# Kernel optimization log

Hardware: AMD Instinct MI355X
Metric: run time of the kernel (lower is better)

Reference implementation:

```python
import jax, jax.numpy as jnp
import numpy as np

N, H, T, L, D_IN, D_QK, D_V = 8, 8, 1024, 1024, 128, 128, 128


def setup_inputs() -> dict:
    key = jax.random.key(0)
    ks = jax.random.split(key, 12)
    s = 1.0 / np.sqrt(D_IN)
    sq = 1.0 / np.sqrt(D_QK)
    return {
        "X": jax.random.normal(ks[0], (N, H, L, D_IN), jnp.float32),
        "t1": jax.random.normal(ks[1], (N, T), jnp.float32),
        "Q": jax.random.normal(ks[2], (N, H, T, D_QK), jnp.float32),
        "Wk1": jax.random.normal(ks[3], (D_IN, D_QK), jnp.float32) * s,
        "bk1": jnp.zeros((D_QK,), jnp.float32),
        "Wk2": jax.random.normal(ks[4], (D_QK, D_QK), jnp.float32) * sq,
        "bk2": jnp.zeros((D_QK,), jnp.float32),
        "Wv1": jax.random.normal(ks[5], (D_IN, D_QK), jnp.float32) * s,
        "bv1": jnp.zeros((D_QK,), jnp.float32),
        "Wv2": jax.random.normal(ks[6], (D_QK, D_V), jnp.float32) * sq,
        "bv2": jnp.zeros((D_V,), jnp.float32),
        "log_tau": jnp.asarray(0.0, jnp.float32),  # log(init_tau=1)
    }


def _mlp(x, W1, b1, W2, b2):
    # MLP(d_in, [d_qk], d_out): Linear -> relu -> Linear
    return jax.nn.relu(x @ W1 + b1) @ W2 + b2


def reference(X, t1, Q, Wk1, bk1, Wk2, bk2, Wv1, bv1, Wv2, bv2, log_tau):
    t2 = X[:, 0, :, -1]                      # (N, L)
    K = _mlp(X, Wk1, bk1, Wk2, bk2)          # (N, H, L, d_qk)
    V = _mlp(X, Wv1, bv1, Wv2, bv2)          # (N, H, L, d_v)
    tau = jnp.exp(log_tau)
    # gaussian weight: -(Q.K)^2 / tau
    A = jnp.einsum('nhtc,nhlc->nhtl', Q, K)
    A = -(A * A) / tau
    mask = (t1[:, :, None] >= t2[:, None, :])[:, None, :, :]  # (N,1,T,L)
    A = jax.nn.softmax(A * mask, axis=-1) * mask
    return jnp.einsum('nhtl,nhlc->nhtc', A, V)
```

## Files before the change

### kernel.cpp

```cpp
#include <hip/hip_runtime.h>
#include <hip/hip_bf16.h>

typedef __bf16 bf16_t;
typedef _Float16 f16_t;
typedef bf16_t bf16x8 __attribute__((ext_vector_type(8)));
typedef f16_t  f16x8  __attribute__((ext_vector_type(8)));
typedef f16_t  f16x4  __attribute__((ext_vector_type(4)));
typedef float  floatx4 __attribute__((ext_vector_type(4)));
typedef float  floatx16 __attribute__((ext_vector_type(16)));
typedef bf16x8 bf16x8u __attribute__((aligned(8)));
typedef f16x8  f16x8u  __attribute__((aligned(8)));

#define DEV static __device__ __forceinline__

DEV floatx4 mfma16_bf16(bf16x8 a, bf16x8 b, floatx4 c) {
  return __builtin_amdgcn_mfma_f32_16x16x32_bf16(a, b, c, 0, 0, 0);
}
DEV floatx4 mfma16_f16(f16x8 a, f16x8 b, floatx4 c) {
  return __builtin_amdgcn_mfma_f32_16x16x32_f16(a, b, c, 0, 0, 0);
}
DEV floatx16 mfma32_bf16(bf16x8 a, bf16x8 b, floatx16 c) {
  return __builtin_amdgcn_mfma_f32_32x32x16_bf16(a, b, c, 0, 0, 0);
}
DEV floatx16 mfma32x8_f16(f16x4 a, f16x4 b, floatx16 c) {
  return __builtin_amdgcn_mfma_f32_32x32x8f16(a, b, c, 0, 0, 0);
}
DEV void async_ld16(void* lds, const void* g) {
  __builtin_amdgcn_global_load_lds(
      (const __attribute__((address_space(1))) unsigned int*)g,
      (__attribute__((address_space(3))) unsigned int*)lds, 16, 0, 0);
}
DEV float fast_exp2(float x) {
  float r;
  asm("v_exp_f32 %0, %1" : "=v"(r) : "v"(x));
  return r;
}

__global__ void prep_kernel(const float* __restrict__ Wk1, const float* __restrict__ Wk2,
                            const float* __restrict__ Wv1, const float* __restrict__ Wv2,
                            const float* __restrict__ X,
                            bf16_t* __restrict__ W1p, bf16_t* __restrict__ W2p,
                            f16_t* __restrict__ W3f, f16_t* __restrict__ W4f,
                            float* __restrict__ t2pre) {
  int b = blockIdx.x;
  if (b < 16) {
    int m = b >> 2, p = b & 3;
    const float* src = m == 0 ? Wk1 : m == 1 ? Wk2 : m == 2 ? Wv1 : Wv2;
    __shared__ float tile[32][129];
    for (int u = 0; u < 4; ++u) {
      int idx = threadIdx.x + u * 256;
      int k = idx >> 5, n4 = (idx & 31) << 2;
      float4 v = *(const float4*)(src + (size_t)(p * 32 + k) * 128 + n4);
      tile[k][n4 + 0] = v.x; tile[k][n4 + 1] = v.y;
      tile[k][n4 + 2] = v.z; tile[k][n4 + 3] = v.w;
    }
    __syncthreads();
    if (m < 2) {
      bf16_t* dst = m ? W2p : W1p;
      for (int u = 0; u < 2; ++u) {
        int idx = threadIdx.x + u * 256;
        int n = idx >> 2, kc = idx & 3;
        bf16x8 hi, lo;
        for (int j = 0; j < 8; ++j) {
          float v = tile[kc * 8 + j][n];
          bf16_t hh = (bf16_t)v;
          hi[j] = hh;
          lo[j] = (bf16_t)(v - (float)hh);
        }
        *(bf16x8*)(dst + n * 128 + p * 32 + kc * 8) = hi;
        *(bf16x8*)(dst + 16384 + n * 128 + p * 32 + kc * 8) = lo;
      }
    } else {
      f16_t* dst = (m == 3) ? W4f : W3f;
      for (int u = 0; u < 2; ++u) {
        int idx = threadIdx.x + u * 256;
        int n = idx >> 2, kc = idx & 3;
        f16x8 w;
        for (int j = 0; j < 8; ++j) w[j] = (f16_t)tile[kc * 8 + j][n];
        *(f16x8*)(dst + n * 128 + p * 32 + kc * 8) = w;
      }
    }
  } else {
    int i = (b - 16) * 256 + threadIdx.x;
    t2pre[i] = X[((size_t)(i >> 10) * 8192 + (i & 1023)) * 128 + 127];
  }
}

__global__ __launch_bounds__(256) void mlp_k_kernel(
    const float* __restrict__ X, const float* __restrict__ b1,
    const float* __restrict__ b2, const bf16_t* __restrict__ W1p,
    const bf16_t* __restrict__ W2p, bf16_t* __restrict__ Khi,
    bf16_t* __restrict__ Klo) {
  __shared__ __align__(16) char sXbuf[2 * 16896];
  __shared__ __align__(16) bf16_t sW[2][256 * 40];
  bf16_t* sXh = (bf16_t*)sXbuf;
  bf16_t* sXl = sXh + 64 * 132;

  const int tid = threadIdx.x, lane = tid & 63, wave = tid >> 6;
  const int q = lane >> 4, c15 = lane & 15;
  const size_t rowBase = (size_t)blockIdx.x * 64;

  int goff[5];
  for (int a = 0; a < 5; ++a) {
    int o = (wave + 4 * a) * 1024 + lane * 16;
    int row = o / 80, rem = o % 80;
    goff[a] = row * 256 + (rem < 64 ? rem : 0);
  }
  auto issueW = [&](int buf, int ph) {
    const bf16_t* Wp = (ph < 4) ? W1p : W2p;
    const char* base = (const char*)Wp + (ph & 3) * 64;
    for (int a = 0; a < 5; ++a)
      async_ld16((char*)sW[buf] + (wave + 4 * a) * 1024 + lane * 16, base + goff[a]);
  };

  issueW(0, 0);

  float b1v[8], b2v[8];
  for (int nt = 0; nt < 8; ++nt) { b1v[nt] = b1[nt * 16 + c15]; b2v[nt] = b2[nt * 16 + c15]; }

  for (int u = 0; u < 8; ++u) {
    int idx = tid + u * 256;
    int r = idx >> 5, c4 = (idx & 31) << 2;
    float4 v = *(const float4*)(X + (rowBase + r) * 128 + c4);
    int o = r * 132 + c4;
    float vv[4] = {v.x, v.y, v.z, v.w};
    for (int i = 0; i < 4; ++i) {
      bf16_t h = (bf16_t)vv[i];
      sXh[o + i] = h;
      sXl[o + i] = (bf16_t)(vv[i] - (float)h);
    }
  }

  floatx4 acc1[8], acc2[8];
  for (int i = 0; i < 8; ++i) { acc1[i] = {}; acc2[i] = {}; }

  __syncthreads();
#pragma unroll
  for (int ph = 0; ph < 8; ++ph) {
    if (ph < 7) issueW((ph + 1) & 1, ph + 1);
    const bf16_t* wb = sW[ph & 1];
    const int kq = ph & 3;
    floatx4* acc = (ph < 4) ? acc1 : acc2;
    const int ao = (wave * 16 + c15) * 132 + kq * 32 + q * 8;
    bf16x8 ah = *(const bf16x8u*)(sXh + ao);
    bf16x8 al = *(const bf16x8u*)(sXl + ao);
    for (int nt = 0; nt < 8; ++nt) {
      const int bo = (nt * 16 + c15) * 40 + q * 8;
      bf16x8 bh = *(const bf16x8*)(wb + bo);
      bf16x8 bl = *(const bf16x8*)(wb + 128 * 40 + bo);
      acc[nt] = mfma16_bf16(ah, bh, acc[nt]);
      acc[nt] = mfma16_bf16(ah, bl, acc[nt]);
      acc[nt] = mfma16_bf16(al, bh, acc[nt]);
    }
    if (ph == 3) {
      for (int nt = 0; nt < 8; ++nt)
        for (int r = 0; r < 4; ++r) {
          float h = fmaxf(acc1[nt][r] + b1v[nt], 0.f);
          bf16_t hh = (bf16_t)h;
          int o = (wave * 16 + q * 4 + r) * 132 + nt * 16 + c15;
          sXh[o] = hh;
          sXl[o] = (bf16_t)(h - (float)hh);
        }
    }
    __syncthreads();
  }

  for (int nt = 0; nt < 8; ++nt)
    for (int r = 0; r < 4; ++r) {
      float kv = acc2[nt][r] + b2v[nt];
      bf16_t kh = (bf16_t)kv;
      int o = (wave * 16 + q * 4 + r) * 132 + nt * 16 + c15;
      sXh[o] = kh;
      sXl[o] = (bf16_t)(kv - (float)kh);
    }
  __syncthreads();
  for (int u = 0; u < 4; ++u) {
    int idx = tid + u * 256;
    int r = idx >> 4, c8 = (idx & 15) << 3;
    bf16x8 vh = *(const bf16x8u*)(sXh + r * 132 + c8);
    bf16x8 vl = *(const bf16x8u*)(sXl + r * 132 + c8);
    *(bf16x8*)(Khi + (rowBase + r) * 128 + c8) = vh;
    *(bf16x8*)(Klo + (rowBase + r) * 128 + c8) = vl;
  }
}

__global__ __launch_bounds__(256) void mlp_v_kernel(
    const float* __restrict__ X, const float* __restrict__ b1,
    const float* __restrict__ b2, const f16_t* __restrict__ W1f,
    const f16_t* __restrict__ W2f, f16_t* __restrict__ Vt) {
  __shared__ __align__(16) f16_t sXf[64 * 136];
  __shared__ __align__(16) f16_t sW[2][128 * 40];

  const int tid = threadIdx.x, lane = tid & 63, wave = tid >> 6;
  const int q = lane >> 4, c15 = lane & 15;
  const size_t rowBase = (size_t)blockIdx.x * 64;

  int goff[3];
  for (int a = 0; a < 3; ++a) {
    int o = (wave + 4 * a) * 1024 + lane * 16;
    int row = o / 80, rem = o % 80;
    goff[a] = row * 256 + (rem < 64 ? rem : 0);
  }
  auto issueV = [&](int buf, int ph) {
    const f16_t* Wp = (ph < 4) ? W1f : W2f;
    const char* base = (const char*)Wp + (ph & 3) * 64;
    for (int a = 0; a < 3; ++a) {
      int j = wave + 4 * a;
      if (j < 10) async_ld16((char*)sW[buf] + j * 1024 + lane * 16, base + goff[a]);
    }
  };

  issueV(0, 0);

  float b1v[8], bvv[2][4];
  for (int nt = 0; nt < 8; ++nt) b1v[nt] = b1[nt * 16 + c15];
  for (int mt = 0; mt < 2; ++mt)
    for (int r = 0; r < 4; ++r)
      bvv[mt][r] = b2[(wave * 2 + mt) * 16 + q * 4 + r];

  for (int u = 0; u < 8; ++u) {
    int idx = tid + u * 256;
    int r = idx >> 5, c4 = (idx & 31) << 2;
    float4 v = *(const float4*)(X + (rowBase + r) * 128 + c4);
    int o = r * 136 + c4;
    sXf[o + 0] = (f16_t)v.x; sXf[o + 1] = (f16_t)v.y;
    sXf[o + 2] = (f16_t)v.z; sXf[o + 3] = (f16_t)v.w;
  }

  floatx4 acc1[8], acc2[2][4];
  for (int i = 0; i < 8; ++i) acc1[i] = {};
  for (int i = 0; i < 2; ++i) for (int j = 0; j < 4; ++j) acc2[i][j] = {};

  __syncthreads();
#pragma unroll
  for (int ph = 0; ph < 8; ++ph) {
    if (ph < 7) issueV((ph + 1) & 1, ph + 1);
    const f16_t* wb = sW[ph & 1];
    const int kq = ph & 3;
    if (ph < 4) {
      f16x8 a = *(const f16x8u*)(sXf + (wave * 16 + c15) * 136 + kq * 32 + q * 8);
      for (int nt = 0; nt < 8; ++nt) {
        f16x8 bb = *(const f16x8*)(wb + (nt * 16 + c15) * 40 + q * 8);
        acc1[nt] = mfma16_f16(a, bb, acc1[nt]);
      }
      if (ph == 3) {
        for (int nt = 0; nt < 8; ++nt)
          for (int r = 0; r < 4; ++r)
            sXf[(wave * 16 + q * 4 + r) * 136 + nt * 16 + c15] =
                (f16_t)fmaxf(acc1[nt][r] + b1v[nt], 0.f);
      }
    } else {
      f16x8 aw0 = *(const f16x8*)(wb + ((wave * 2 + 0) * 16 + c15) * 40 + q * 8);
      f16x8 aw1 = *(const f16x8*)(wb + ((wave * 2 + 1) * 16 + c15) * 40 + q * 8);
      for (int nt = 0; nt < 4; ++nt) {
        f16x8 bh = *(const f16x8u*)(sXf + (nt * 16 + c15) * 136 + kq * 32 + q * 8);
        acc2[0][nt] = mfma16_f16(aw0, bh, acc2[0][nt]);
        acc2[1][nt] = mfma16_f16(aw1, bh, acc2[1][nt]);
      }
    }
    __syncthreads();
  }

  f16_t* sVT = sXf;
  for (int mt = 0; mt < 2; ++mt)
    for (int nt = 0; nt < 4; ++nt)
      for (int r = 0; r < 4; ++r) {
        int c = (wave * 2 + mt) * 16 + q * 4 + r;
        sVT[c * 68 + nt * 16 + c15] = (f16_t)(acc2[mt][nt][r] + bvv[mt][r]);
      }
  __syncthreads();
  const int nh = (int)(rowBase >> 10);
  const int lB = (int)(rowBase & 1023);
  for (int u = 0; u < 4; ++u) {
    int idx = tid + u * 256;
    int c = idx >> 3, l8 = (idx & 7) << 3;
    *(f16x8*)(Vt + ((size_t)nh * 128 + c) * 1024 + lB + l8) =
        *(const f16x8u*)(sVT + c * 68 + l8);
  }
}

__global__ __launch_bounds__(256, 2) void attn_kernel(
    const float* __restrict__ Q, const float* __restrict__ t1,
    const float* __restrict__ t2pre, const float* __restrict__ ltau,
    const bf16_t* __restrict__ Khi, const bf16_t* __restrict__ Klo,
    const f16_t* __restrict__ Vt, float* __restrict__ out) {
  __shared__ __align__(16) char sBuf[3][24576];
  __shared__ __align__(16) float sT2[1024];

  const int tid = threadIdx.x, lane = tid & 63, wave = tid >> 6;
  const int h = lane >> 5, l31 = lane & 31;
  const int nh = blockIdx.x & 63;
  const int seg = blockIdx.x >> 6;
  const int n = nh >> 3;
  const int qrow = seg * 128 + wave * 32 + l31;
  const float negc2 = -__expf(-ltau[0]) * 1.44269504f;
  const int vswz = (l31 >> 1) & 3;

  const char* gp[6]; int ls[6]; int st[6];
  for (int a = 0; a < 6; ++a) {
    int j = wave + 4 * a;
    if (j < 16) {
      int o = j * 1024 + lane * 16;
      int half = o >> 13;
      int r2 = o & 8191;
      int row = r2 >> 8;
      int s = (r2 >> 4) & 15;
      int g = s ^ (row & 15);
      gp[a] = (const char*)(half ? Klo : Khi) +
              ((size_t)((nh << 10) + row)) * 256 + (g << 4);
      st[a] = 8192; ls[a] = o;
    } else {
      int o = (j - 16) * 1024 + lane * 16;
      int c = o >> 6;
      int u = (o >> 4) & 3;
      int up = u ^ ((c >> 1) & 3);
      gp[a] = (const char*)Vt + ((size_t)((nh << 7) + c)) * 2048 + up * 16;
      st[a] = 64; ls[a] = 16384 + o;
    }
  }
  auto stage = [&](int buf) {
    for (int a = 0; a < 6; ++a) { async_ld16(sBuf[buf] + ls[a], gp[a]); gp[a] += st[a]; }
  };

  float4 t2v4 = *(const float4*)(t2pre + (n << 10) + tid * 4);
  const float t1v = t1[(n << 10) + qrow];
  bf16x8 qh[8], ql[8];
  {
    const float* qr = Q + ((size_t)(nh << 10) + qrow) * 128;
    for (int ks = 0; ks < 8; ++ks) {
      const float* p = qr + ks * 16 + h * 8;
      float4 v0 = *(const float4*)p;
      float4 v1 = *(const float4*)(p + 4);
      float vv[8] = {v0.x, v0.y, v0.z, v0.w, v1.x, v1.y, v1.z, v1.w};
      bf16x8 hi, lo;
      for (int j = 0; j < 8; ++j) {
        bf16_t hj = (bf16_t)vv[j];
        hi[j] = hj;
        lo[j] = (bf16_t)(vv[j] - (float)hj);
      }
      qh[ks] = hi;
      ql[ks] = lo;
    }
  }
  stage(0);
  stage(1);
  *(float4*)(sT2 + tid * 4) = t2v4;

  floatx16 O[4];
  for (int i = 0; i < 4; ++i) O[i] = {};
  float ds = 0.f;

  asm volatile("s_waitcnt vmcnt(6) lgkmcnt(0)" ::: "memory");
  __builtin_amdgcn_s_barrier();
  asm volatile("" ::: "memory");

  for (int it = 0; it < 32; ++it) {
    if (it <= 29) stage((it + 2) % 3);
    const char* kb = sBuf[it % 3];
    const char* vb = kb + 16384;

    floatx16 S = {};
    __builtin_amdgcn_s_setprio(1);
#pragma unroll
    for (int ks = 0; ks < 8; ++ks) {
      const int bo = l31 * 256 + ((((ks << 1) + h) ^ (l31 & 15)) << 4);
      bf16x8 kh_ = *(const bf16x8*)(kb + bo);
      bf16x8 kl_ = *(const bf16x8*)(kb + 8192 + bo);
      S = mfma32_bf16(kh_, qh[ks], S);
      S = mfma32_bf16(kl_, qh[ks], S);
      S = mfma32_bf16(kh_, ql[ks], S);
    }
    __builtin_amdgcn_s_setprio(0);

    const float* t2b = sT2 + it * 32 + h * 4;
    for (int t = 0; t < 4; ++t) {
      float4 tv4 = *(const float4*)(t2b + t * 8);
      float tv[4] = {tv4.x, tv4.y, tv4.z, tv4.w};
      f16x4 pb;
      for (int j = 0; j < 4; ++j) {
        float s = S[4 * t + j];
        float e = fast_exp2(s * s * negc2);
        bool m = (t1v >= tv[j]);
        ds += m ? e : 1.f;
        pb[j] = (f16_t)(m ? e : 0.f);
      }
      for (int ct = 0; ct < 4; ++ct) {
        f16x4 va = *(const f16x4*)(vb + (ct * 32 + l31) * 64 +
                                   ((t ^ vswz) << 4) + h * 8);
        O[ct] = mfma32x8_f16(va, pb, O[ct]);
      }
    }

    if (it <= 29) {
      asm volatile("s_waitcnt vmcnt(6)" ::: "memory");
    } else if (it == 30) {
      asm volatile("s_waitcnt vmcnt(0)" ::: "memory");
    }
    if (it < 31) {
      asm volatile("" ::: "memory");
      __builtin_amdgcn_s_barrier();
      asm volatile("" ::: "memory");
    }
  }

  ds += __shfl_xor(ds, 32);
  const float inv = 1.f / ds;
  float* orow = out + ((size_t)(nh << 10) + qrow) * 128;
  for (int ct = 0; ct < 4; ++ct)
    for (int t = 0; t < 4; ++t) {
      int c = ct * 32 + 8 * t + 4 * h;
      float4 v = {O[ct][4 * t + 0] * inv, O[ct][4 * t + 1] * inv,
                  O[ct][4 * t + 2] * inv, O[ct][4 * t + 3] * inv};
      *(float4*)(orow + c) = v;
    }
}

extern "C" void kernel_launch(void* const* d_in, const int* in_sizes, int n_in,
                              void* d_out, int out_size, void* d_ws, size_t ws_size,
                              hipStream_t stream) {
  const float* X   = (const float*)d_in[0];
  const float* t1  = (const float*)d_in[1];
  const float* Q   = (const float*)d_in[2];
  const float* Wk1 = (const float*)d_in[3];
  const float* bk1 = (const float*)d_in[4];
  const float* Wk2 = (const float*)d_in[5];
  const float* bk2 = (const float*)d_in[6];
  const float* Wv1 = (const float*)d_in[7];
  const float* bv1 = (const float*)d_in[8];
  const float* Wv2 = (const float*)d_in[9];
  const float* bv2 = (const float*)d_in[10];
  const float* log_tau = (const float*)d_in[11];
  float* out = (float*)d_out;

  const size_t E = (size_t)64 * 1024 * 128;
  bf16_t* Khi = (bf16_t*)d_ws;
  bf16_t* Klo = Khi + E;
  f16_t*  Vt  = (f16_t*)(Klo + E);
  bf16_t* W1p = (bf16_t*)((char*)d_ws + 3 * E * 2);
  bf16_t* W2p = W1p + 32768;
  f16_t*  W3f = (f16_t*)(W2p + 32768);
  f16_t*  W4f = W3f + 16384;
  float*  t2pre = (float*)(W4f + 16384);

  prep_kernel<<<48, 256, 0, stream>>>(Wk1, Wk2, Wv1, Wv2, X, W1p, W2p, W3f, W4f, t2pre);
  mlp_k_kernel<<<1024, 256, 0, stream>>>(X, bk1, bk2, W1p, W2p, Khi, Klo);
  mlp_v_kernel<<<1024, 256, 0, stream>>>(X, bv1, bv2, W3f, W4f, Vt);
  attn_kernel<<<512, 256, 0, stream>>>(Q, t1, t2pre, log_tau, Khi, Klo, Vt, out);
}
```

Before: 230.3 us.

## Switch attention kernel to 16x16 MFMA tiles with 8 waves per block

The attention kernel moves from 32x32 MFMA tiles (one 32-query tile per wave, 4 waves) to 16x16 MFMA tiles (16 queries per wave, 8 waves per 512-thread block). The async staging work is spread across 8 waves with 3 loads each, and the V LDS swizzle is changed to match the new access pattern. Launch bounds change to 512 threads with a target of 4 blocks. The aim is more waves per CU to hide latency and smaller per-wave accumulators. The cost is more LDS reads of K and V per MFMA, since each 16x16 tile gets less operand reuse.

```diff
diff --git a/kernel.cpp b/kernel.cpp
--- a/kernel.cpp
+++ b/kernel.cpp
@@ -19,11 +19,8 @@
 DEV floatx4 mfma16_f16(f16x8 a, f16x8 b, floatx4 c) {
   return __builtin_amdgcn_mfma_f32_16x16x32_f16(a, b, c, 0, 0, 0);
 }
-DEV floatx16 mfma32_bf16(bf16x8 a, bf16x8 b, floatx16 c) {
-  return __builtin_amdgcn_mfma_f32_32x32x16_bf16(a, b, c, 0, 0, 0);
-}
-DEV floatx16 mfma32x8_f16(f16x4 a, f16x4 b, floatx16 c) {
-  return __builtin_amdgcn_mfma_f32_32x32x8f16(a, b, c, 0, 0, 0);
+DEV floatx4 mfma16x16_f16(f16x4 a, f16x4 b, floatx4 c) {
+  return __builtin_amdgcn_mfma_f32_16x16x16f16(a, b, c, 0, 0, 0);
 }
 DEV void async_ld16(void* lds, const void* g) {
   __builtin_amdgcn_global_load_lds(
@@ -279,7 +276,7 @@
   }
 }
 
-__global__ __launch_bounds__(256, 2) void attn_kernel(
+__global__ __launch_bounds__(512, 4) void attn_kernel(
     const float* __restrict__ Q, const float* __restrict__ t1,
     const float* __restrict__ t2pre, const float* __restrict__ ltau,
     const bf16_t* __restrict__ Khi, const bf16_t* __restrict__ Klo,
@@ -288,17 +285,16 @@
   __shared__ __align__(16) float sT2[1024];
 
   const int tid = threadIdx.x, lane = tid & 63, wave = tid >> 6;
-  const int h = lane >> 5, l31 = lane & 31;
+  const int q = lane >> 4, r15 = lane & 15;
   const int nh = blockIdx.x & 63;
   const int seg = blockIdx.x >> 6;
   const int n = nh >> 3;
-  const int qrow = seg * 128 + wave * 32 + l31;
+  const int qbase = seg * 128 + wave * 16;
   const float negc2 = -__expf(-ltau[0]) * 1.44269504f;
-  const int vswz = (l31 >> 1) & 3;
-
-  const char* gp[6]; int ls[6]; int st[6];
-  for (int a = 0; a < 6; ++a) {
-    int j = wave + 4 * a;
+
+  const char* gp[3]; int ls[3]; int st[3];
+  for (int a = 0; a < 3; ++a) {
+    int j = wave + 8 * a;
     if (j < 16) {
       int o = j * 1024 + lane * 16;
       int half = o >> 13;
@@ -311,24 +307,24 @@
       st[a] = 8192; ls[a] = o;
     } else {
       int o = (j - 16) * 1024 + lane * 16;
-      int c = o >> 6;
+      int d = o >> 6;
       int u = (o >> 4) & 3;
-      int up = u ^ ((c >> 1) & 3);
-      gp[a] = (const char*)Vt + ((size_t)((nh << 7) + c)) * 2048 + up * 16;
+      int up = u ^ (d & 3);
+      gp[a] = (const char*)Vt + ((size_t)((nh << 7) + d)) * 2048 + (up << 4);
       st[a] = 64; ls[a] = 16384 + o;
     }
   }
   auto stage = [&](int buf) {
-    for (int a = 0; a < 6; ++a) { async_ld16(sBuf[buf] + ls[a], gp[a]); gp[a] += st[a]; }
+    for (int a = 0; a < 3; ++a) { async_ld16(sBuf[buf] + ls[a], gp[a]); gp[a] += st[a]; }
   };
 
-  float4 t2v4 = *(const float4*)(t2pre + (n << 10) + tid * 4);
-  const float t1v = t1[(n << 10) + qrow];
-  bf16x8 qh[8], ql[8];
+  float2 t2v2 = *(const float2*)(t2pre + (n << 10) + tid * 2);
+  const float t1v = t1[(n << 10) + qbase + r15];
+  bf16x8 qh[4], ql[4];
   {
-    const float* qr = Q + ((size_t)(nh << 10) + qrow) * 128;
-    for (int ks = 0; ks < 8; ++ks) {
-      const float* p = qr + ks * 16 + h * 8;
+    const float* qr = Q + ((size_t)(nh << 10) + qbase + r15) * 128;
+    for (int kq = 0; kq < 4; ++kq) {
+      const float* p = qr + kq * 32 + q * 8;
       float4 v0 = *(const float4*)p;
       float4 v1 = *(const float4*)(p + 4);
       float vv[8] = {v0.x, v0.y, v0.z, v0.w, v1.x, v1.y, v1.z, v1.w};
@@ -338,19 +334,19 @@
         hi[j] = hj;
         lo[j] = (bf16_t)(vv[j] - (float)hj);
       }
-      qh[ks] = hi;
-      ql[ks] = lo;
+      qh[kq] = hi;
+      ql[kq] = lo;
     }
   }
   stage(0);
   stage(1);
-  *(float4*)(sT2 + tid * 4) = t2v4;
-
-  floatx16 O[4];
-  for (int i = 0; i < 4; ++i) O[i] = {};
+  *(float2*)(sT2 + tid * 2) = t2v2;
+
+  floatx4 O[8];
+  for (int i = 0; i < 8; ++i) O[i] = {};
   float ds = 0.f;
 
-  asm volatile("s_waitcnt vmcnt(6) lgkmcnt(0)" ::: "memory");
+  asm volatile("s_waitcnt vmcnt(3) lgkmcnt(0)" ::: "memory");
   __builtin_amdgcn_s_barrier();
   asm volatile("" ::: "memory");
 
@@ -359,40 +355,51 @@
     const char* kb = sBuf[it % 3];
     const char* vb = kb + 16384;
 
-    floatx16 S = {};
+    floatx4 Sa = {}, Sb = {};
     __builtin_amdgcn_s_setprio(1);
 #pragma unroll
-    for (int ks = 0; ks < 8; ++ks) {
-      const int bo = l31 * 256 + ((((ks << 1) + h) ^ (l31 & 15)) << 4);
-      bf16x8 kh_ = *(const bf16x8*)(kb + bo);
-      bf16x8 kl_ = *(const bf16x8*)(kb + 8192 + bo);
-      S = mfma32_bf16(kh_, qh[ks], S);
-      S = mfma32_bf16(kl_, qh[ks], S);
-      S = mfma32_bf16(kh_, ql[ks], S);
+    for (int kq = 0; kq < 4; ++kq) {
+      const int un = (((kq << 2) + q) ^ r15) << 4;
+      const int boA = r15 * 256 + un;
+      const int boB = (16 + r15) * 256 + un;
+      bf16x8 kha = *(const bf16x8*)(kb + boA);
+      bf16x8 kla = *(const bf16x8*)(kb + 8192 + boA);
+      bf16x8 khb = *(const bf16x8*)(kb + boB);
+      bf16x8 klb = *(const bf16x8*)(kb + 8192 + boB);
+      Sa = mfma16_bf16(kha, qh[kq], Sa);
+      Sa = mfma16_bf16(kla, qh[kq], Sa);
+      Sa = mfma16_bf16(kha, ql[kq], Sa);
+      Sb = mfma16_bf16(khb, qh[kq], Sb);
+      Sb = mfma16_bf16(klb, qh[kq], Sb);
+      Sb = mfma16_bf16(khb, ql[kq], Sb);
     }
     __builtin_amdgcn_s_setprio(0);
 
-    const float* t2b = sT2 + it * 32 + h * 4;
-    for (int t = 0; t < 4; ++t) {
-      float4 tv4 = *(const float4*)(t2b + t * 8);
+    const float* t2b = sT2 + it * 32 + 4 * q;
+#pragma unroll
+    for (int c1 = 0; c1 < 2; ++c1) {
+      floatx4 Sv = c1 ? Sb : Sa;
+      float4 tv4 = *(const float4*)(t2b + c1 * 16);
       float tv[4] = {tv4.x, tv4.y, tv4.z, tv4.w};
       f16x4 pb;
       for (int j = 0; j < 4; ++j) {
-        float s = S[4 * t + j];
+        float s = Sv[j];
         float e = fast_exp2(s * s * negc2);
         bool m = (t1v >= tv[j]);
         ds += m ? e : 1.f;
         pb[j] = (f16_t)(m ? e : 0.f);
       }
-      for (int ct = 0; ct < 4; ++ct) {
-        f16x4 va = *(const f16x4*)(vb + (ct * 32 + l31) * 64 +
-                                   ((t ^ vswz) << 4) + h * 8);
-        O[ct] = mfma32x8_f16(va, pb, O[ct]);
+      const int v = q + (c1 << 2);
+      const int vo = (((v >> 1) ^ (r15 & 3)) << 4) + ((v & 1) << 3);
+#pragma unroll
+      for (int dt = 0; dt < 8; ++dt) {
+        f16x4 va = *(const f16x4*)(vb + (dt * 16 + r15) * 64 + vo);
+        O[dt] = mfma16x16_f16(va, pb, O[dt]);
       }
     }
 
     if (it <= 29) {
-      asm volatile("s_waitcnt vmcnt(6)" ::: "memory");
+      asm volatile("s_waitcnt vmcnt(3)" ::: "memory");
     } else if (it == 30) {
       asm volatile("s_waitcnt vmcnt(0)" ::: "memory");
     }
@@ -403,16 +410,15 @@
     }
   }
 
+  ds += __shfl_xor(ds, 16);
   ds += __shfl_xor(ds, 32);
   const float inv = 1.f / ds;
-  float* orow = out + ((size_t)(nh << 10) + qrow) * 128;
-  for (int ct = 0; ct < 4; ++ct)
-    for (int t = 0; t < 4; ++t) {
-      int c = ct * 32 + 8 * t + 4 * h;
-      float4 v = {O[ct][4 * t + 0] * inv, O[ct][4 * t + 1] * inv,
-                  O[ct][4 * t + 2] * inv, O[ct][4 * t + 3] * inv};
-      *(float4*)(orow + c) = v;
-    }
+  float* orow = out + ((size_t)(nh << 10) + qbase + r15) * 128;
+#pragma unroll
+  for (int dt = 0; dt < 8; ++dt) {
+    float4 v = {O[dt][0] * inv, O[dt][1] * inv, O[dt][2] * inv, O[dt][3] * inv};
+    *(float4*)(orow + dt * 16 + 4 * q) = v;
+  }
 }
 
 extern "C" void kernel_launch(void* const* d_in, const int* in_sizes, int n_in,
@@ -445,5 +451,5 @@
   prep_kernel<<<48, 256, 0, stream>>>(Wk1, Wk2, Wv1, Wv2, X, W1p, W2p, W3f, W4f, t2pre);
   mlp_k_kernel<<<1024, 256, 0, stream>>>(X, bk1, bk2, W1p, W2p, Khi, Klo);
   mlp_v_kernel<<<1024, 256, 0, stream>>>(X, bv1, bv2, W3f, W4f, Vt);
-  attn_kernel<<<512, 256, 0, stream>>>(Q, t1, t2pre, log_tau, Khi, Klo, Vt, out);
-}
+  attn_kernel<<<512, 512, 0, stream>>>(Q, t1, t2pre, log_tau, Khi, Klo, Vt, out);
+}
```

After: 247.4 us. 7.4% more time.

## Store V in MFMA fragment layout and load it directly into registers

Applied to the files above, without the earlier changes.

The V MLP kernel now writes V in a layout that matches the per-lane MFMA A-fragment order for each 32-row tile. The attention kernel loads those fragments from global memory straight into registers instead of staging V through shared memory. This shrinks the LDS ring buffers to K only, and the launch bound is raised to 3 blocks per CU to get more occupancy. In exchange, each iteration adds 16 direct global loads per lane and register pressure goes up, which could spill or stall on global-load latency now that V is no longer pipelined through async copies.

```diff
diff --git a/kernel.cpp b/kernel.cpp
--- a/kernel.cpp
+++ b/kernel.cpp
@@ -187,7 +187,7 @@
 __global__ __launch_bounds__(256) void mlp_v_kernel(
     const float* __restrict__ X, const float* __restrict__ b1,
     const float* __restrict__ b2, const f16_t* __restrict__ W1f,
-    const f16_t* __restrict__ W2f, f16_t* __restrict__ Vt) {
+    const f16_t* __restrict__ W2f, f16_t* __restrict__ Vf) {
   __shared__ __align__(16) f16_t sXf[64 * 136];
   __shared__ __align__(16) f16_t sW[2][128 * 40];
 
@@ -269,22 +269,27 @@
         sVT[c * 68 + nt * 16 + c15] = (f16_t)(acc2[mt][nt][r] + bvv[mt][r]);
       }
   __syncthreads();
-  const int nh = (int)(rowBase >> 10);
-  const int lB = (int)(rowBase & 1023);
-  for (int u = 0; u < 4; ++u) {
-    int idx = tid + u * 256;
-    int c = idx >> 3, l8 = (idx & 7) << 3;
-    *(f16x8*)(Vt + ((size_t)nh * 128 + c) * 1024 + lB + l8) =
-        *(const f16x8u*)(sVT + c * 68 + l8);
-  }
-}
-
-__global__ __launch_bounds__(256, 2) void attn_kernel(
+  const int nhV = (int)(rowBase >> 10);
+  const int itB = (int)((rowBase & 1023) >> 5);
+  char* vfB = (char*)Vf + (((size_t)nhV * 32 + itB) << 13);
+  for (int u = 0; u < 8; ++u) {
+    int idx = u * 256 + tid;
+    int itl = idx >> 10;
+    int f   = (idx >> 6) & 15;
+    int l   = idx & 63;
+    int d   = (f >> 2) * 32 + (l & 31);
+    int Ll  = itl * 32 + (f & 3) * 8 + ((l >> 5) << 2);
+    f16x4 v = *(const f16x4*)(sVT + d * 68 + Ll);
+    *(f16x4*)(vfB + (size_t)((((itl << 4) + f) << 9) + (l << 3))) = v;
+  }
+}
+
+__global__ __launch_bounds__(256, 3) void attn_kernel(
     const float* __restrict__ Q, const float* __restrict__ t1,
     const float* __restrict__ t2pre, const float* __restrict__ ltau,
     const bf16_t* __restrict__ Khi, const bf16_t* __restrict__ Klo,
-    const f16_t* __restrict__ Vt, float* __restrict__ out) {
-  __shared__ __align__(16) char sBuf[3][24576];
+    const f16_t* __restrict__ Vf, float* __restrict__ out) {
+  __shared__ __align__(16) char sBuf[3][16384];
   __shared__ __align__(16) float sT2[1024];
 
   const int tid = threadIdx.x, lane = tid & 63, wave = tid >> 6;
@@ -294,32 +299,22 @@
   const int n = nh >> 3;
   const int qrow = seg * 128 + wave * 32 + l31;
   const float negc2 = -__expf(-ltau[0]) * 1.44269504f;
-  const int vswz = (l31 >> 1) & 3;
-
-  const char* gp[6]; int ls[6]; int st[6];
-  for (int a = 0; a < 6; ++a) {
+
+  const char* gp[4]; int ls[4];
+  for (int a = 0; a < 4; ++a) {
     int j = wave + 4 * a;
-    if (j < 16) {
-      int o = j * 1024 + lane * 16;
-      int half = o >> 13;
-      int r2 = o & 8191;
-      int row = r2 >> 8;
-      int s = (r2 >> 4) & 15;
-      int g = s ^ (row & 15);
-      gp[a] = (const char*)(half ? Klo : Khi) +
-              ((size_t)((nh << 10) + row)) * 256 + (g << 4);
-      st[a] = 8192; ls[a] = o;
-    } else {
-      int o = (j - 16) * 1024 + lane * 16;
-      int c = o >> 6;
-      int u = (o >> 4) & 3;
-      int up = u ^ ((c >> 1) & 3);
-      gp[a] = (const char*)Vt + ((size_t)((nh << 7) + c)) * 2048 + up * 16;
-      st[a] = 64; ls[a] = 16384 + o;
-    }
+    int o = j * 1024 + lane * 16;
+    int half = o >> 13;
+    int r2 = o & 8191;
+    int row = r2 >> 8;
+    int s = (r2 >> 4) & 15;
+    int g = s ^ (row & 15);
+    gp[a] = (const char*)(half ? Klo : Khi) +
+            ((size_t)((nh << 10) + row)) * 256 + (g << 4);
+    ls[a] = o;
   }
   auto stage = [&](int buf) {
-    for (int a = 0; a < 6; ++a) { async_ld16(sBuf[buf] + ls[a], gp[a]); gp[a] += st[a]; }
+    for (int a = 0; a < 4; ++a) { async_ld16(sBuf[buf] + ls[a], gp[a]); gp[a] += 8192; }
   };
 
   float4 t2v4 = *(const float4*)(t2pre + (n << 10) + tid * 4);
@@ -346,18 +341,23 @@
   stage(1);
   *(float4*)(sT2 + tid * 4) = t2v4;
 
+  const char* vfb = (const char*)Vf + ((size_t)nh << 18) + lane * 8;
+
   floatx16 O[4];
   for (int i = 0; i < 4; ++i) O[i] = {};
   float ds = 0.f;
 
-  asm volatile("s_waitcnt vmcnt(6) lgkmcnt(0)" ::: "memory");
+  asm volatile("s_waitcnt vmcnt(4) lgkmcnt(0)" ::: "memory");
   __builtin_amdgcn_s_barrier();
   asm volatile("" ::: "memory");
 
   for (int it = 0; it < 32; ++it) {
+    const char* vtb = vfb + ((size_t)it << 13);
+    f16x4 vr[16];
+#pragma unroll
+    for (int f = 0; f < 16; ++f) vr[f] = *(const f16x4*)(vtb + (f << 9));
     if (it <= 29) stage((it + 2) % 3);
     const char* kb = sBuf[it % 3];
-    const char* vb = kb + 16384;
 
     floatx16 S = {};
     __builtin_amdgcn_s_setprio(1);
@@ -373,6 +373,7 @@
     __builtin_amdgcn_s_setprio(0);
 
     const float* t2b = sT2 + it * 32 + h * 4;
+#pragma unroll
     for (int t = 0; t < 4; ++t) {
       float4 tv4 = *(const float4*)(t2b + t * 8);
       float tv[4] = {tv4.x, tv4.y, tv4.z, tv4.w};
@@ -384,18 +385,11 @@
         ds += m ? e : 1.f;
         pb[j] = (f16_t)(m ? e : 0.f);
       }
-      for (int ct = 0; ct < 4; ++ct) {
-        f16x4 va = *(const f16x4*)(vb + (ct * 32 + l31) * 64 +
-                                   ((t ^ vswz) << 4) + h * 8);
-        O[ct] = mfma32x8_f16(va, pb, O[ct]);
-      }
-    }
-
-    if (it <= 29) {
-      asm volatile("s_waitcnt vmcnt(6)" ::: "memory");
-    } else if (it == 30) {
-      asm volatile("s_waitcnt vmcnt(0)" ::: "memory");
-    }
+#pragma unroll
+      for (int ct = 0; ct < 4; ++ct)
+        O[ct] = mfma32x8_f16(vr[ct * 4 + t], pb, O[ct]);
+    }
+
     if (it < 31) {
       asm volatile("" ::: "memory");
       __builtin_amdgcn_s_barrier();
@@ -406,6 +400,7 @@
   ds += __shfl_xor(ds, 32);
   const float inv = 1.f / ds;
   float* orow = out + ((size_t)(nh << 10) + qrow) * 128;
+#pragma unroll
   for (int ct = 0; ct < 4; ++ct)
     for (int t = 0; t < 4; ++t) {
       int c = ct * 32 + 8 * t + 4 * h;
@@ -435,7 +430,7 @@
   const size_t E = (size_t)64 * 1024 * 128;
   bf16_t* Khi = (bf16_t*)d_ws;
   bf16_t* Klo = Khi + E;
-  f16_t*  Vt  = (f16_t*)(Klo + E);
+  f16_t*  Vf  = (f16_t*)(Klo + E);
   bf16_t* W1p = (bf16_t*)((char*)d_ws + 3 * E * 2);
   bf16_t* W2p = W1p + 32768;
   f16_t*  W3f = (f16_t*)(W2p + 32768);
@@ -444,6 +439,6 @@
 
   prep_kernel<<<48, 256, 0, stream>>>(Wk1, Wk2, Wv1, Wv2, X, W1p, W2p, W3f, W4f, t2pre);
   mlp_k_kernel<<<1024, 256, 0, stream>>>(X, bk1, bk2, W1p, W2p, Khi, Klo);
-  mlp_v_kernel<<<1024, 256, 0, stream>>>(X, bv1, bv2, W3f, W4f, Vt);
-  attn_kernel<<<512, 256, 0, stream>>>(Q, t1, t2pre, log_tau, Khi, Klo, Vt, out);
-}
+  mlp_v_kernel<<<1024, 256, 0, stream>>>(X, bv1, bv2, W3f, W4f, Vf);
+  attn_kernel<<<512, 256, 0, stream>>>(Q, t1, t2pre, log_tau, Khi, Klo, Vf, out);
+}
```

Measured after the change: 352.4 us. 53.0% more time.

## Software-pipeline QK for next tile with softmax and PV of current tile

Applied to the files above, without the earlier changes.

Restructures the attention loop so the QK^T MFMAs for tile it+1 are issued while the exp/mask and PV MFMAs for tile it run, with a peeled prologue and epilogue. V fragments are preloaded into registers and the inner loops are fully unrolled. The launch bound drops the 2-blocks-per-CU hint, and the wait before each barrier becomes vmcnt(0) instead of vmcnt(6). That stricter wait may give up some of the 3-stage prefetch depth. The extra live registers (Sn, vr) may reduce occupancy.

```diff
diff --git a/kernel.cpp b/kernel.cpp
--- a/kernel.cpp
+++ b/kernel.cpp
@@ -279,7 +279,7 @@
   }
 }
 
-__global__ __launch_bounds__(256, 2) void attn_kernel(
+__global__ __launch_bounds__(256) void attn_kernel(
     const float* __restrict__ Q, const float* __restrict__ t1,
     const float* __restrict__ t2pre, const float* __restrict__ ltau,
     const bf16_t* __restrict__ Khi, const bf16_t* __restrict__ Klo,
@@ -350,17 +350,13 @@
   for (int i = 0; i < 4; ++i) O[i] = {};
   float ds = 0.f;
 
-  asm volatile("s_waitcnt vmcnt(6) lgkmcnt(0)" ::: "memory");
+  asm volatile("s_waitcnt vmcnt(0) lgkmcnt(0)" ::: "memory");
   __builtin_amdgcn_s_barrier();
   asm volatile("" ::: "memory");
 
-  for (int it = 0; it < 32; ++it) {
-    if (it <= 29) stage((it + 2) % 3);
-    const char* kb = sBuf[it % 3];
-    const char* vb = kb + 16384;
-
-    floatx16 S = {};
-    __builtin_amdgcn_s_setprio(1);
+  floatx16 S = {};
+  {
+    const char* kb = sBuf[0];
 #pragma unroll
     for (int ks = 0; ks < 8; ++ks) {
       const int bo = l31 * 256 + ((((ks << 1) + h) ^ (l31 & 15)) << 4);
@@ -370,9 +366,36 @@
       S = mfma32_bf16(kl_, qh[ks], S);
       S = mfma32_bf16(kh_, ql[ks], S);
     }
+  }
+
+  for (int it = 0; it < 31; ++it) {
+    if (it <= 29) stage((it + 2) % 3);
+
+    const char* vb = sBuf[it % 3] + 16384;
+    f16x4 vr[16];
+#pragma unroll
+    for (int ct = 0; ct < 4; ++ct)
+#pragma unroll
+      for (int t = 0; t < 4; ++t)
+        vr[ct * 4 + t] = *(const f16x4*)(vb + (ct * 32 + l31) * 64 +
+                                         ((t ^ vswz) << 4) + h * 8);
+
+    const char* kbn = sBuf[(it + 1) % 3];
+    floatx16 Sn = {};
+    __builtin_amdgcn_s_setprio(1);
+#pragma unroll
+    for (int ks = 0; ks < 8; ++ks) {
+      const int bo = l31 * 256 + ((((ks << 1) + h) ^ (l31 & 15)) << 4);
+      bf16x8 kh_ = *(const bf16x8*)(kbn + bo);
+      bf16x8 kl_ = *(const bf16x8*)(kbn + 8192 + bo);
+      Sn = mfma32_bf16(kh_, qh[ks], Sn);
+      Sn = mfma32_bf16(kl_, qh[ks], Sn);
+      Sn = mfma32_bf16(kh_, ql[ks], Sn);
+    }
     __builtin_amdgcn_s_setprio(0);
 
     const float* t2b = sT2 + it * 32 + h * 4;
+#pragma unroll
     for (int t = 0; t < 4; ++t) {
       float4 tv4 = *(const float4*)(t2b + t * 8);
       float tv[4] = {tv4.x, tv4.y, tv4.z, tv4.w};
@@ -384,28 +407,48 @@
         ds += m ? e : 1.f;
         pb[j] = (f16_t)(m ? e : 0.f);
       }
+#pragma unroll
+      for (int ct = 0; ct < 4; ++ct)
+        O[ct] = mfma32x8_f16(vr[ct * 4 + t], pb, O[ct]);
+    }
+    S = Sn;
+
+    if (it <= 29) {
+      asm volatile("s_waitcnt vmcnt(0)" ::: "memory");
+      asm volatile("" ::: "memory");
+      __builtin_amdgcn_s_barrier();
+      asm volatile("" ::: "memory");
+    }
+  }
+
+  {
+    const char* vb = sBuf[31 % 3] + 16384;
+    const float* t2b = sT2 + 31 * 32 + h * 4;
+#pragma unroll
+    for (int t = 0; t < 4; ++t) {
+      float4 tv4 = *(const float4*)(t2b + t * 8);
+      float tv[4] = {tv4.x, tv4.y, tv4.z, tv4.w};
+      f16x4 pb;
+      for (int j = 0; j < 4; ++j) {
+        float s = S[4 * t + j];
+        float e = fast_exp2(s * s * negc2);
+        bool m = (t1v >= tv[j]);
+        ds += m ? e : 1.f;
+        pb[j] = (f16_t)(m ? e : 0.f);
+      }
+#pragma unroll
       for (int ct = 0; ct < 4; ++ct) {
         f16x4 va = *(const f16x4*)(vb + (ct * 32 + l31) * 64 +
                                    ((t ^ vswz) << 4) + h * 8);
         O[ct] = mfma32x8_f16(va, pb, O[ct]);
       }
     }
-
-    if (it <= 29) {
-      asm volatile("s_waitcnt vmcnt(6)" ::: "memory");
-    } else if (it == 30) {
-      asm volatile("s_waitcnt vmcnt(0)" ::: "memory");
-    }
-    if (it < 31) {
-      asm volatile("" ::: "memory");
-      __builtin_amdgcn_s_barrier();
-      asm volatile("" ::: "memory");
-    }
   }
 
   ds += __shfl_xor(ds, 32);
   const float inv = 1.f / ds;
   float* orow = out + ((size_t)(nh << 10) + qrow) * 128;
+#pragma unroll
   for (int ct = 0; ct < 4; ++ct)
     for (int t = 0; t < 4; ++t) {
       int c = ct * 32 + 8 * t + 4 * h;
```

Result: slower. 268.1 us (+16.4%).
